# Optimization experiments

Measured on AMD Instinct MI355X. Metric: run time of the kernel, lower is better.

## Reference

```python
import jax, jax.numpy as jnp
import numpy as np


def _linear_init(key, fan_in, fan_out):
    bound = 1.0 / np.sqrt(fan_in)
    k1, k2 = jax.random.split(key)
    w = jax.random.uniform(k1, (fan_in, fan_out), jnp.float32, -bound, bound)
    b = jax.random.uniform(k2, (fan_out,), jnp.float32, -bound, bound)
    return w, b


def setup_inputs() -> dict:
    key = jax.random.key(0)
    ks = jax.random.split(key, 8)
    B, T, K, F, H, D = 4, 64, 50, 6, 128, 256
    states = jax.random.normal(ks[0], (B, T, K, F), jnp.float32)
    masks = (jax.random.uniform(ks[1], (B, T, K)) < 0.9).astype(jnp.float32)
    w_a, b_a = _linear_init(ks[2], F, H)              # agent_encoder
    w_r1, b_r1 = _linear_init(ks[3], 2 * H + 3, H)    # relation_encoder layer 1
    w_r2, b_r2 = _linear_init(ks[4], H, H)            # relation_encoder layer 2
    w_g, b_g = _linear_init(ks[5], 2 * H, H)          # graph_aggregation
    w_f1, b_f1 = _linear_init(ks[6], H, D)            # final_encoder layer 1
    w_f2, b_f2 = _linear_init(ks[7], D, D)            # final_encoder layer 2
    return dict(states=states, masks=masks, w_a=w_a, b_a=b_a,
                w_r1=w_r1, b_r1=b_r1, w_r2=w_r2, b_r2=b_r2,
                w_g=w_g, b_g=b_g, w_f1=w_f1, b_f1=b_f1, w_f2=w_f2, b_f2=b_f2)


def _safe_norm(r):
    # sqrt(sum r^2) with well-defined gradient at 0 (torch.norm convention)
    sq = jnp.sum(r * r, axis=-1, keepdims=True)
    return jnp.where(sq == 0, 0.0, jnp.sqrt(jnp.where(sq == 0, 1.0, sq)))


def reference(states, masks, w_a, b_a, w_r1, b_r1, w_r2, b_r2,
              w_g, b_g, w_f1, b_f1, w_f2, b_f2):
    B, T, K, F = states.shape
    H = w_a.shape[1]
    s = states.reshape(B * T, K, F)            # [N,K,F]
    m = masks.reshape(B * T, K)                # [N,K]
    agent_feat = jax.nn.relu(s @ w_a + b_a)    # [N,K,H] (dropout = identity, eval)
    pos = s[..., :2]
    vel = s[..., 2:4]
    # rel[n,i,j] = quantity_j - quantity_i
    rel_pos = pos[:, None, :, :] - pos[:, :, None, :]   # [N,K,K,2]
    rel_vel = vel[:, None, :, :] - vel[:, :, None, :]
    dist = _safe_norm(rel_pos)                          # [N,K,K,1]
    rx, ry = rel_pos[..., 0:1], rel_pos[..., 1:2]
    safe_x = jnp.where((rx == 0) & (ry == 0), 1.0, rx)  # atan2(0,1)=atan2(0,0)=0
    angle = jnp.arctan2(ry, safe_x)
    speed_diff = _safe_norm(rel_vel)
    geo = jnp.concatenate([dist, angle, speed_diff], axis=-1)  # [N,K,K,3]
    # Split the first relation linear instead of materializing the
    # [N,K,K,2H+3] concat: cat([f_i, f_j, geo]) @ w_r1 == f@w_i + f@w_j + geo@w_geo
    x_i = agent_feat @ w_r1[:H]            # [N,K,H]
    x_j = agent_feat @ w_r1[H:2 * H]       # [N,K,H]
    g = geo @ w_r1[2 * H:] + b_r1          # [N,K,K,H]
    h = jax.nn.relu(x_i[:, :, None, :] + x_j[:, None, :, :] + g)
    rel_feat = h @ w_r2 + b_r2             # [N,K,K,H]
    mask_pairs = m[:, :, None] * m[:, None, :]          # [N,i,j]
    rel_feat = rel_feat * mask_pairs[..., None]
    denom = jnp.maximum(mask_pairs.sum(axis=2, keepdims=True), 1.0)  # [N,K,1]
    agg = rel_feat.sum(axis=2) / denom                  # [N,K,H]
    combined = jax.nn.relu(agent_feat @ w_g[:H] + agg @ w_g[H:] + b_g)  # [N,K,H]
    me = m[..., None]
    pooled = (combined * me).sum(axis=1) / jnp.maximum(me.sum(axis=1), 1.0)  # [N,H]
    latent = jax.nn.relu(pooled @ w_f1 + b_f1) @ w_f2 + b_f2                 # [N,D]
    return latent.reshape(B, T, -1)
```

## Files before the change

kernel.cpp:

```cpp
#include <hip/hip_runtime.h>

#define KA 50
#define KP 52
#define H 128
#define D 256
#define NBLK 256
#define BLOCK 1024
#define NG 8
#define RPT 7
#define STRD 136

#define WS_WI 0
#define WS_WJ 32
#define WS_WR2 64
#define WS_WG 96
#define NFRAG 160

typedef __attribute__((ext_vector_type(8))) short bf16x8;
typedef __attribute__((ext_vector_type(4))) float f32x4;
typedef __attribute__((ext_vector_type(2))) float v2f;

__device__ __forceinline__ float bf2f(unsigned short u) {
  return __uint_as_float(((unsigned)u) << 16);
}
__device__ __forceinline__ unsigned short f2bf_rne(float f) {
  unsigned u = __float_as_uint(f);
  u = (u + 0x7FFFu + ((u >> 16) & 1u)) >> 16;
  return (unsigned short)u;
}
__device__ __forceinline__ unsigned short f2bf(float f) {
  return (unsigned short)((__float_as_uint(f) + 0x8000u) >> 16);
}
__device__ __forceinline__ int rli(int v, int l) {
  return __builtin_amdgcn_readlane(v, l);
}
__device__ __forceinline__ float fast_atan2(float y, float x) {
  const float ax = fabsf(x), ay = fabsf(y);
  const float mx = fmaxf(ax, ay), mn = fminf(ax, ay);
  const float r  = mn * __builtin_amdgcn_rcpf(mx);
  const float r2 = r * r;
  float p = fmaf(r2, 0.0208351f, -0.0851330f);
  p = fmaf(r2, p, 0.1801410f);
  p = fmaf(r2, p, -0.3302995f);
  p = fmaf(r2, p, 0.9998660f);
  float th = r * p;
  if (ay > ax) th = 1.57079632679f - th;
  if (x < 0.f) th = 3.14159265359f - th;
  return copysignf(th, y);
}

__global__ void pack_weights(const float* __restrict__ w_r1,
                             const float* __restrict__ w_r2,
                             const float* __restrict__ w_g,
                             unsigned short* __restrict__ wp) {
  const int t = blockIdx.x * 256 + threadIdx.x;
  if (t >= NFRAG * 64) return;
  const int f = t >> 6, lane = t & 63;
  const float* W; int rowbase, sf;
  if (f < 64)       { W = w_r1; rowbase = (f < 32) ? 0 : 128; sf = f & 31; }
  else if (f < 96)  { W = w_r2; rowbase = 0; sf = f - 64; }
  else              { W = w_g;  rowbase = 0; sf = f - 96; }
  const int kt = sf >> 3, ctl = sf & 7;
  const int col = ctl * 16 + (lane & 15);
  const int k0  = rowbase + kt * 32 + (lane >> 4) * 8;
  unsigned short v[8];
  #pragma unroll
  for (int j = 0; j < 8; ++j) v[j] = f2bf_rne(W[(k0 + j) * H + col]);
  #pragma unroll
  for (int j = 0; j < 8; ++j) wp[(size_t)t * 8 + j] = v[j];
}

struct alignas(16) Smem {
  unsigned short af[KP * STRD];
  unsigned short xi[KP * STRD];
  unsigned short xj[KP * H];
  unsigned short hsum[KP * STRD];
  float red[1024];
  float pooled[H];
  float latent1[D];
  float s[KA][6];
  float m[64];
  float cnta[KP];
  float invden[KP];
  float cnt;
};

__global__ void __launch_bounds__(BLOCK) rpe_kernel(
    const float* __restrict__ states, const float* __restrict__ masks,
    const float* __restrict__ w_a,  const float* __restrict__ b_a,
    const float* __restrict__ w_r1, const float* __restrict__ b_r1,
    const float* __restrict__ b_r2,
    const float* __restrict__ b_g,
    const float* __restrict__ w_f1, const float* __restrict__ b_f1,
    const float* __restrict__ w_f2, const float* __restrict__ b_f2,
    const unsigned short* __restrict__ wp,
    float* __restrict__ out) {
  __shared__ Smem sh;
  const int n = blockIdx.x;
  const int tid = threadIdx.x;
  const int c = tid & (H - 1);
  const int bg = tid >> 7;
  const int wid = tid >> 6, lane = tid & 63;
  const int ct = wid & 7;
  const int rtb = (wid >> 3) * 2;
  const int fr = lane & 15;
  const int fkg = lane >> 4;
  const int col = ct * 16 + fr;

  const float bac = b_a[c];
  const float wa0 = w_a[0*H+c], wa1 = w_a[1*H+c], wa2 = w_a[2*H+c];
  const float wa3 = w_a[3*H+c], wa4 = w_a[4*H+c], wa5 = w_a[5*H+c];
  const int c0 = 2 * lane;
  const v2f wgd01  = { w_r1[256*H + c0], w_r1[256*H + c0+1] };
  const v2f wgan01 = { w_r1[257*H + c0], w_r1[257*H + c0+1] };
  const v2f wgs01  = { w_r1[258*H + c0], w_r1[258*H + c0+1] };
  const v2f br101  = { b_r1[c0], b_r1[c0+1] };

  {
    if (tid < KA * 6) ((float*)sh.s)[tid] = states[(size_t)n * (KA * 6) + tid];
    if (tid < 64) sh.m[tid] = (tid < KA) ? masks[(size_t)n * KA + tid] : 0.f;
    if (tid < 2 * H) {
      const int r5 = KA + (tid >> 7), cc = tid & (H - 1);
      sh.af[r5 * STRD + cc] = 0;
      sh.hsum[r5 * STRD + cc] = 0;
    }
  }
  __syncthreads();
  if (wid == 0) {
    float v = sh.m[lane];
    v += __shfl_xor(v, 1);  v += __shfl_xor(v, 2);  v += __shfl_xor(v, 4);
    v += __shfl_xor(v, 8);  v += __shfl_xor(v, 16); v += __shfl_xor(v, 32);
    if (lane == 0) sh.cnt = v;
  }

  const int bl = (lane < KA) ? lane : (KA - 1);
  const float pbx = sh.s[bl][0], pby = sh.s[bl][1];
  const float pvx = sh.s[bl][2], pvy = sh.s[bl][3];
  const unsigned mbits = (sh.m[lane] != 0.f) ? 0x3F800000u : 0u;
  unsigned q0[3], q1[3];
  #pragma unroll
  for (int r = 0; r < 3; ++r) {
    const int ar = wid + 16 * r;
    const float rx  = pbx - sh.s[ar][0], ry  = pby - sh.s[ar][1];
    const float dvx = pvx - sh.s[ar][2], dvy = pvy - sh.s[ar][3];
    const float dist = sqrtf(fmaf(rx, rx, ry * ry));
    const float sx = (rx == 0.f && ry == 0.f) ? 1.f : rx;
    const float ang = fast_atan2(ry, sx);
    const float sd  = sqrtf(fmaf(dvx, dvx, dvy * dvy));
    q0[r] = (unsigned)f2bf(dist) | ((unsigned)f2bf(ang) << 16);
    q1[r] = (unsigned)f2bf(sd) | mbits;
  }
  unsigned q0t = 0, q1t = 0;
  if (wid < 2) {
    const int ar = 48 + wid;
    const float rx  = pbx - sh.s[ar][0], ry  = pby - sh.s[ar][1];
    const float dvx = pvx - sh.s[ar][2], dvy = pvy - sh.s[ar][3];
    const float dist = sqrtf(fmaf(rx, rx, ry * ry));
    const float sx = (rx == 0.f && ry == 0.f) ? 1.f : rx;
    const float ang = fast_atan2(ry, sx);
    const float sd  = sqrtf(fmaf(dvx, dvx, dvy * dvy));
    q0t = (unsigned)f2bf(dist) | ((unsigned)f2bf(ang) << 16);
    q1t = (unsigned)f2bf(sd) | mbits;
  }

  {
    #pragma unroll
    for (int r = 0; r < RPT; ++r) {
      const int a = bg + NG * r;
      if (a < KA) {
        const float* srow = sh.s[a];
        float v = fmaf(srow[0], wa0, fmaf(srow[1], wa1, fmaf(srow[2], wa2,
                  fmaf(srow[3], wa3, fmaf(srow[4], wa4, fmaf(srow[5], wa5, bac))))));
        sh.af[a * STRD + c] = f2bf(fmaxf(v, 0.f));
      }
    }
  }
  bf16x8 Bi[4], Bj[4];
  #pragma unroll
  for (int kt = 0; kt < 4; ++kt) {
    Bi[kt] = *(const bf16x8*)&wp[(size_t)((WS_WI + kt*8 + ct) * 64 + lane) * 8];
    Bj[kt] = *(const bf16x8*)&wp[(size_t)((WS_WJ + kt*8 + ct) * 64 + lane) * 8];
  }
  __syncthreads();
  if (tid < KP) {
    const float ca = (tid < KA) ? sh.m[tid] * sh.cnt : 0.f;
    sh.cnta[tid] = ca;
    sh.invden[tid] = 1.0f / fmaxf(ca, 1.0f);
  }

  {
    f32x4 ci0 = {0,0,0,0}, ci1 = {0,0,0,0}, cj0 = {0,0,0,0}, cj1 = {0,0,0,0};
    #pragma unroll
    for (int kt = 0; kt < 4; ++kt) {
      const bf16x8 A0 = *(const bf16x8*)&sh.af[(rtb*16 + fr) * STRD + kt*32 + fkg*8];
      const bf16x8 A1 = *(const bf16x8*)&sh.af[((rtb+1)*16 + fr) * STRD + kt*32 + fkg*8];
      ci0 = __builtin_amdgcn_mfma_f32_16x16x32_bf16(A0, Bi[kt], ci0, 0, 0, 0);
      ci1 = __builtin_amdgcn_mfma_f32_16x16x32_bf16(A1, Bi[kt], ci1, 0, 0, 0);
      cj0 = __builtin_amdgcn_mfma_f32_16x16x32_bf16(A0, Bj[kt], cj0, 0, 0, 0);
      cj1 = __builtin_amdgcn_mfma_f32_16x16x32_bf16(A1, Bj[kt], cj1, 0, 0, 0);
    }
    #pragma unroll
    for (int rt2 = 0; rt2 < 2; ++rt2) {
      const f32x4 vi = rt2 ? ci1 : ci0;
      const f32x4 vj = rt2 ? cj1 : cj0;
      #pragma unroll
      for (int g = 0; g < 4; ++g) {
        const int r = (rtb + rt2) * 16 + fkg * 4 + g;
        if (r < KP) {
          sh.xi[r * STRD + col] = f2bf(vi[g]);
          sh.xj[r * H + col]    = f2bf(vj[g]);
        }
      }
    }
  }
  __syncthreads();

  {
    v2f base01[3], acc01[3];
    #pragma unroll
    for (int r = 0; r < 3; ++r) {
      const int ar = wid + 16 * r;
      const unsigned xip = *(const unsigned*)&sh.xi[ar * STRD + c0];
      base01[r] = (v2f){ bf2f((unsigned short)xip), bf2f((unsigned short)(xip >> 16)) } + br101;
      acc01[r] = (v2f){0.f, 0.f};
    }
    #pragma unroll 10
    for (int b = 0; b < KA; ++b) {
      const unsigned xjp = *(const unsigned*)&sh.xj[b * H + c0];
      const v2f xj01 = { __uint_as_float(xjp << 16),
                         __uint_as_float(xjp & 0xFFFF0000u) };
      #pragma unroll
      for (int r = 0; r < 3; ++r) {
        const unsigned rq0 = (unsigned)rli((int)q0[r], b);
        const unsigned rq1 = (unsigned)rli((int)q1[r], b);
        const float dd = __uint_as_float(rq0 << 16);
        const float aa = __uint_as_float(rq0 & 0xFFFF0000u);
        const float ss = __uint_as_float(rq1 << 16);
        const float mm = __uint_as_float(rq1 & 0xFFFF0000u);
        v2f t = __builtin_elementwise_fma((v2f){dd, dd}, wgd01, base01[r] + xj01);
        t = __builtin_elementwise_fma((v2f){aa, aa}, wgan01, t);
        t = __builtin_elementwise_fma((v2f){ss, ss}, wgs01, t);
        t = __builtin_elementwise_max(t, (v2f){0.f, 0.f});
        acc01[r] = __builtin_elementwise_fma((v2f){mm, mm}, t, acc01[r]);
      }
    }
    #pragma unroll
    for (int r = 0; r < 3; ++r) {
      const int ar = wid + 16 * r;
      const float ma = sh.m[ar];
      *(unsigned*)&sh.hsum[ar * STRD + c0] =
          (unsigned)f2bf(acc01[r].x * ma) | ((unsigned)f2bf(acc01[r].y * ma) << 16);
    }
    if (wid < 2) {
      const int ar = 48 + wid;
      const unsigned xip = *(const unsigned*)&sh.xi[ar * STRD + c0];
      const v2f baset = (v2f){ bf2f((unsigned short)xip),
                               bf2f((unsigned short)(xip >> 16)) } + br101;
      v2f acct = {0.f, 0.f};
      #pragma unroll 10
      for (int b = 0; b < KA; ++b) {
        const unsigned xjp = *(const unsigned*)&sh.xj[b * H + c0];
        const v2f xj01 = { __uint_as_float(xjp << 16),
                           __uint_as_float(xjp & 0xFFFF0000u) };
        const unsigned rq0 = (unsigned)rli((int)q0t, b);
        const unsigned rq1 = (unsigned)rli((int)q1t, b);
        const float dd = __uint_as_float(rq0 << 16);
        const float aa = __uint_as_float(rq0 & 0xFFFF0000u);
        const float ss = __uint_as_float(rq1 << 16);
        const float mm = __uint_as_float(rq1 & 0xFFFF0000u);
        v2f t = __builtin_elementwise_fma((v2f){dd, dd}, wgd01, baset + xj01);
        t = __builtin_elementwise_fma((v2f){aa, aa}, wgan01, t);
        t = __builtin_elementwise_fma((v2f){ss, ss}, wgs01, t);
        t = __builtin_elementwise_max(t, (v2f){0.f, 0.f});
        acct = __builtin_elementwise_fma((v2f){mm, mm}, t, acct);
      }
      const float ma = sh.m[ar];
      *(unsigned*)&sh.hsum[ar * STRD + c0] =
          (unsigned)f2bf(acct.x * ma) | ((unsigned)f2bf(acct.y * ma) << 16);
    }
  }
  __syncthreads();

  f32x4 p0 = {0,0,0,0}, p1 = {0,0,0,0};
  {
    f32x4 a0 = {0,0,0,0}, a1 = {0,0,0,0};
    #pragma unroll
    for (int kt = 0; kt < 4; ++kt) {
      const bf16x8 B4 = *(const bf16x8*)&wp[(size_t)((WS_WR2 + kt*8 + ct) * 64 + lane) * 8];
      const bf16x8 A0h = *(const bf16x8*)&sh.hsum[(rtb*16 + fr) * STRD + kt*32 + fkg*8];
      const bf16x8 A1h = *(const bf16x8*)&sh.hsum[((rtb+1)*16 + fr) * STRD + kt*32 + fkg*8];
      a0 = __builtin_amdgcn_mfma_f32_16x16x32_bf16(A0h, B4, a0, 0, 0, 0);
      a1 = __builtin_amdgcn_mfma_f32_16x16x32_bf16(A1h, B4, a1, 0, 0, 0);
      const bf16x8 B5 = *(const bf16x8*)&wp[(size_t)((WS_WG + kt*8 + ct) * 64 + lane) * 8];
      const bf16x8 A0a = *(const bf16x8*)&sh.af[(rtb*16 + fr) * STRD + kt*32 + fkg*8];
      const bf16x8 A1a = *(const bf16x8*)&sh.af[((rtb+1)*16 + fr) * STRD + kt*32 + fkg*8];
      p0 = __builtin_amdgcn_mfma_f32_16x16x32_bf16(A0a, B5, p0, 0, 0, 0);
      p1 = __builtin_amdgcn_mfma_f32_16x16x32_bf16(A1a, B5, p1, 0, 0, 0);
    }
    const float br2c = b_r2[col];
    #pragma unroll
    for (int rt2 = 0; rt2 < 2; ++rt2) {
      const f32x4 v = rt2 ? a1 : a0;
      #pragma unroll
      for (int g = 0; g < 4; ++g) {
        const int r = (rtb + rt2) * 16 + fkg * 4 + g;
        if (r < KP) {
          const float val = fmaf(sh.cnta[r], br2c, v[g]) * sh.invden[r];
          sh.xi[r * STRD + col] = f2bf(val);
        }
      }
    }
  }
  __syncthreads();

  {
    #pragma unroll
    for (int kt = 0; kt < 4; ++kt) {
      const bf16x8 B = *(const bf16x8*)&wp[(size_t)((WS_WG + (kt+4)*8 + ct) * 64 + lane) * 8];
      const bf16x8 A0 = *(const bf16x8*)&sh.xi[(rtb*16 + fr) * STRD + kt*32 + fkg*8];
      const bf16x8 A1 = *(const bf16x8*)&sh.xi[((rtb+1)*16 + fr) * STRD + kt*32 + fkg*8];
      p0 = __builtin_amdgcn_mfma_f32_16x16x32_bf16(A0, B, p0, 0, 0, 0);
      p1 = __builtin_amdgcn_mfma_f32_16x16x32_bf16(A1, B, p1, 0, 0, 0);
    }
    const float bgc = b_g[col];
    float pv = 0.f;
    #pragma unroll
    for (int rt2 = 0; rt2 < 2; ++rt2) {
      const f32x4 v = rt2 ? p1 : p0;
      #pragma unroll
      for (int g = 0; g < 4; ++g) {
        const int r = (rtb + rt2) * 16 + fkg * 4 + g;
        if (r < KA) {
          pv = fmaf(sh.m[r], fmaxf(v[g] + bgc, 0.f), pv);
        }
      }
    }
    pv += __shfl_xor(pv, 16);
    pv += __shfl_xor(pv, 32);
    if (lane < 16) sh.red[(wid >> 3) * H + col] = pv;
  }
  __syncthreads();
  if (tid < H) {
    const float invp = 1.0f / fmaxf(sh.cnt, 1.0f);
    sh.pooled[tid] = (sh.red[tid] + sh.red[H + tid]) * invp;
  }
  __syncthreads();

  {
    const int d  = tid & (D - 1);
    const int hh = tid >> 8;
    const float* wf = w_f1 + d;
    float acc = 0.f;
    const int k0 = hh * 32;
    #pragma unroll 8
    for (int k = 0; k < 32; ++k)
      acc = fmaf(sh.pooled[k0 + k], wf[(k0 + k) * D], acc);
    sh.red[hh * D + d] = acc;
  }
  __syncthreads();
  if (tid < D) {
    sh.latent1[tid] = fmaxf(sh.red[tid] + sh.red[D + tid] +
                            sh.red[2*D + tid] + sh.red[3*D + tid] +
                            b_f1[tid], 0.f);
  }
  __syncthreads();

  {
    const int d  = tid & (D - 1);
    const int hh = tid >> 8;
    const float* wf = w_f2 + d;
    float acc = 0.f;
    const int k0 = hh * 64;
    #pragma unroll 8
    for (int k = 0; k < 64; ++k)
      acc = fmaf(sh.latent1[k0 + k], wf[(k0 + k) * D], acc);
    sh.red[hh * D + d] = acc;
  }
  __syncthreads();
  if (tid < D) {
    out[(size_t)n * D + tid] = sh.red[tid] + sh.red[D + tid] +
                               sh.red[2*D + tid] + sh.red[3*D + tid] +
                               b_f2[tid];
  }
}

extern "C" void kernel_launch(void* const* d_in, const int* in_sizes, int n_in,
                              void* d_out, int out_size, void* d_ws, size_t ws_size,
                              hipStream_t stream) {
  const float* states = (const float*)d_in[0];
  const float* masks  = (const float*)d_in[1];
  const float* w_a  = (const float*)d_in[2];
  const float* b_a  = (const float*)d_in[3];
  const float* w_r1 = (const float*)d_in[4];
  const float* b_r1 = (const float*)d_in[5];
  const float* w_r2 = (const float*)d_in[6];
  const float* b_r2 = (const float*)d_in[7];
  const float* w_g  = (const float*)d_in[8];
  const float* b_g  = (const float*)d_in[9];
  const float* w_f1 = (const float*)d_in[10];
  const float* b_f1 = (const float*)d_in[11];
  const float* w_f2 = (const float*)d_in[12];
  const float* b_f2 = (const float*)d_in[13];
  float* out = (float*)d_out;
  unsigned short* wp = (unsigned short*)d_ws;

  hipLaunchKernelGGL(pack_weights, dim3((NFRAG * 64 + 255) / 256), dim3(256), 0, stream,
                     w_r1, w_r2, w_g, wp);
  hipLaunchKernelGGL(rpe_kernel, dim3(NBLK), dim3(BLOCK), 0, stream,
                     states, masks, w_a, b_a, w_r1, b_r1, b_r2,
                     b_g, w_f1, b_f1, w_f2, b_f2, wp, out);
}
```

Baseline: 37.18 us.

## Split tail-row pair loop across eight waves and fold pooled normalization into MLP

The two leftover agent rows (48, 49) used to be handled by two waves looping over all 50 neighbours while the other 14 waves idled. Now 8 waves each take a 12-13 neighbour chunk of one tail row. Their partial sums are reduced through shared memory after an extra barrier. The separate pooled-vector stage and its barrier are also removed by folding the two-way sum and 1/count scale into the first final-encoder matvec, using the xi buffer as scratch.

```diff
diff --git a/kernel.cpp b/kernel.cpp
--- a/kernel.cpp
+++ b/kernel.cpp
@@ -76,7 +76,6 @@
   unsigned short xj[KP * H];
   unsigned short hsum[KP * STRD];
   float red[1024];
-  float pooled[H];
   float latent1[D];
   float s[KA][6];
   float m[64];
@@ -84,6 +83,58 @@
   float invden[KP];
   float cnt;
 };
+
+__device__ __forceinline__ void ph3_main(const Smem& sh, const unsigned* q0,
+                                         const unsigned* q1, const v2f* base01,
+                                         v2f* acc01, v2f wgd01, v2f wgan01,
+                                         v2f wgs01, int c0) {
+  #pragma unroll 10
+  for (int b = 0; b < KA; ++b) {
+    const unsigned xjp = *(const unsigned*)&sh.xj[b * H + c0];
+    const v2f xj01 = { __uint_as_float(xjp << 16),
+                       __uint_as_float(xjp & 0xFFFF0000u) };
+    #pragma unroll
+    for (int r = 0; r < 3; ++r) {
+      const unsigned rq0 = (unsigned)rli((int)q0[r], b);
+      const unsigned rq1 = (unsigned)rli((int)q1[r], b);
+      const float dd = __uint_as_float(rq0 << 16);
+      const float aa = __uint_as_float(rq0 & 0xFFFF0000u);
+      const float ss = __uint_as_float(rq1 << 16);
+      const float mm = __uint_as_float(rq1 & 0xFFFF0000u);
+      v2f t = __builtin_elementwise_fma((v2f){dd, dd}, wgd01, base01[r] + xj01);
+      t = __builtin_elementwise_fma((v2f){aa, aa}, wgan01, t);
+      t = __builtin_elementwise_fma((v2f){ss, ss}, wgs01, t);
+      t = __builtin_elementwise_max(t, (v2f){0.f, 0.f});
+      acc01[r] = __builtin_elementwise_fma((v2f){mm, mm}, t, acc01[r]);
+    }
+  }
+}
+
+template <int LEN>
+__device__ __forceinline__ void ph3_tail(const Smem& sh, int bbeg,
+                                         unsigned q0t, unsigned q1t,
+                                         v2f baset, v2f& acct,
+                                         v2f wgd01, v2f wgan01, v2f wgs01,
+                                         int c0) {
+  #pragma unroll
+  for (int bi = 0; bi < LEN; ++bi) {
+    const int b = bbeg + bi;
+    const unsigned xjp = *(const unsigned*)&sh.xj[b * H + c0];
+    const v2f xj01 = { __uint_as_float(xjp << 16),
+                       __uint_as_float(xjp & 0xFFFF0000u) };
+    const unsigned rq0 = (unsigned)rli((int)q0t, b);
+    const unsigned rq1 = (unsigned)rli((int)q1t, b);
+    const float dd = __uint_as_float(rq0 << 16);
+    const float aa = __uint_as_float(rq0 & 0xFFFF0000u);
+    const float ss = __uint_as_float(rq1 << 16);
+    const float mm = __uint_as_float(rq1 & 0xFFFF0000u);
+    v2f t = __builtin_elementwise_fma((v2f){dd, dd}, wgd01, baset + xj01);
+    t = __builtin_elementwise_fma((v2f){aa, aa}, wgan01, t);
+    t = __builtin_elementwise_fma((v2f){ss, ss}, wgs01, t);
+    t = __builtin_elementwise_max(t, (v2f){0.f, 0.f});
+    acct = __builtin_elementwise_fma((v2f){mm, mm}, t, acct);
+  }
+}
 
 __global__ void __launch_bounds__(BLOCK) rpe_kernel(
     const float* __restrict__ states, const float* __restrict__ masks,
@@ -137,7 +188,11 @@
   const float pbx = sh.s[bl][0], pby = sh.s[bl][1];
   const float pvx = sh.s[bl][2], pvy = sh.s[bl][3];
   const unsigned mbits = (sh.m[lane] != 0.f) ? 0x3F800000u : 0u;
-  unsigned q0[3], q1[3];
+  const bool hastail = (wid < 8);
+  const int ar4 = 48 + (wid & 1);
+  const int chunk = wid >> 1;
+  const int bbeg = (chunk < 2) ? chunk * 13 : 26 + (chunk - 2) * 12;
+  unsigned q0[3], q1[3], q0t = 0, q1t = 0;
   #pragma unroll
   for (int r = 0; r < 3; ++r) {
     const int ar = wid + 16 * r;
@@ -150,9 +205,8 @@
     q0[r] = (unsigned)f2bf(dist) | ((unsigned)f2bf(ang) << 16);
     q1[r] = (unsigned)f2bf(sd) | mbits;
   }
-  unsigned q0t = 0, q1t = 0;
-  if (wid < 2) {
-    const int ar = 48 + wid;
+  if (hastail) {
+    const int ar = ar4;
     const float rx  = pbx - sh.s[ar][0], ry  = pby - sh.s[ar][1];
     const float dvx = pvx - sh.s[ar][2], dvy = pvy - sh.s[ar][3];
     const float dist = sqrtf(fmaf(rx, rx, ry * ry));
@@ -224,26 +278,7 @@
       base01[r] = (v2f){ bf2f((unsigned short)xip), bf2f((unsigned short)(xip >> 16)) } + br101;
       acc01[r] = (v2f){0.f, 0.f};
     }
-    #pragma unroll 10
-    for (int b = 0; b < KA; ++b) {
-      const unsigned xjp = *(const unsigned*)&sh.xj[b * H + c0];
-      const v2f xj01 = { __uint_as_float(xjp << 16),
-                         __uint_as_float(xjp & 0xFFFF0000u) };
-      #pragma unroll
-      for (int r = 0; r < 3; ++r) {
-        const unsigned rq0 = (unsigned)rli((int)q0[r], b);
-        const unsigned rq1 = (unsigned)rli((int)q1[r], b);
-        const float dd = __uint_as_float(rq0 << 16);
-        const float aa = __uint_as_float(rq0 & 0xFFFF0000u);
-        const float ss = __uint_as_float(rq1 << 16);
-        const float mm = __uint_as_float(rq1 & 0xFFFF0000u);
-        v2f t = __builtin_elementwise_fma((v2f){dd, dd}, wgd01, base01[r] + xj01);
-        t = __builtin_elementwise_fma((v2f){aa, aa}, wgan01, t);
-        t = __builtin_elementwise_fma((v2f){ss, ss}, wgs01, t);
-        t = __builtin_elementwise_max(t, (v2f){0.f, 0.f});
-        acc01[r] = __builtin_elementwise_fma((v2f){mm, mm}, t, acc01[r]);
-      }
-    }
+    ph3_main(sh, q0, q1, base01, acc01, wgd01, wgan01, wgs01, c0);
     #pragma unroll
     for (int r = 0; r < 3; ++r) {
       const int ar = wid + 16 * r;
@@ -251,33 +286,24 @@
       *(unsigned*)&sh.hsum[ar * STRD + c0] =
           (unsigned)f2bf(acc01[r].x * ma) | ((unsigned)f2bf(acc01[r].y * ma) << 16);
     }
-    if (wid < 2) {
-      const int ar = 48 + wid;
-      const unsigned xip = *(const unsigned*)&sh.xi[ar * STRD + c0];
+    if (hastail) {
+      const unsigned xip = *(const unsigned*)&sh.xi[ar4 * STRD + c0];
       const v2f baset = (v2f){ bf2f((unsigned short)xip),
                                bf2f((unsigned short)(xip >> 16)) } + br101;
       v2f acct = {0.f, 0.f};
-      #pragma unroll 10
-      for (int b = 0; b < KA; ++b) {
-        const unsigned xjp = *(const unsigned*)&sh.xj[b * H + c0];
-        const v2f xj01 = { __uint_as_float(xjp << 16),
-                           __uint_as_float(xjp & 0xFFFF0000u) };
-        const unsigned rq0 = (unsigned)rli((int)q0t, b);
-        const unsigned rq1 = (unsigned)rli((int)q1t, b);
-        const float dd = __uint_as_float(rq0 << 16);
-        const float aa = __uint_as_float(rq0 & 0xFFFF0000u);
-        const float ss = __uint_as_float(rq1 << 16);
-        const float mm = __uint_as_float(rq1 & 0xFFFF0000u);
-        v2f t = __builtin_elementwise_fma((v2f){dd, dd}, wgd01, baset + xj01);
-        t = __builtin_elementwise_fma((v2f){aa, aa}, wgan01, t);
-        t = __builtin_elementwise_fma((v2f){ss, ss}, wgs01, t);
-        t = __builtin_elementwise_max(t, (v2f){0.f, 0.f});
-        acct = __builtin_elementwise_fma((v2f){mm, mm}, t, acct);
-      }
-      const float ma = sh.m[ar];
-      *(unsigned*)&sh.hsum[ar * STRD + c0] =
-          (unsigned)f2bf(acct.x * ma) | ((unsigned)f2bf(acct.y * ma) << 16);
-    }
+      if (chunk < 2) ph3_tail<13>(sh, bbeg, q0t, q1t, baset, acct, wgd01, wgan01, wgs01, c0);
+      else           ph3_tail<12>(sh, bbeg, q0t, q1t, baset, acct, wgd01, wgan01, wgs01, c0);
+      *(float2*)&sh.red[wid * H + c0] = make_float2(acct.x, acct.y);
+    }
+  }
+  __syncthreads();
+  if (tid < 256) {
+    const int rr = tid >> 7;
+    const int cc = tid & 127;
+    const float v = ((sh.red[rr * H + cc]       + sh.red[(rr + 2) * H + cc]) +
+                     (sh.red[(rr + 4) * H + cc] + sh.red[(rr + 6) * H + cc])) *
+                    sh.m[48 + rr];
+    sh.hsum[(48 + rr) * STRD + cc] = f2bf(v);
   }
   __syncthreads();
 
@@ -340,41 +366,36 @@
     if (lane < 16) sh.red[(wid >> 3) * H + col] = pv;
   }
   __syncthreads();
-  if (tid < H) {
+
+  float* scr = (float*)sh.xi;
+  const int d67 = tid & (D - 1);
+  const int hh67 = tid >> 8;
+  {
     const float invp = 1.0f / fmaxf(sh.cnt, 1.0f);
-    sh.pooled[tid] = (sh.red[tid] + sh.red[H + tid]) * invp;
-  }
-  __syncthreads();
-
-  {
-    const int d  = tid & (D - 1);
-    const int hh = tid >> 8;
-    const float* wf = w_f1 + d;
+    const float* wf = w_f1 + d67;
     float acc = 0.f;
-    const int k0 = hh * 32;
+    const int k0 = hh67 * 32;
     #pragma unroll 8
     for (int k = 0; k < 32; ++k)
-      acc = fmaf(sh.pooled[k0 + k], wf[(k0 + k) * D], acc);
-    sh.red[hh * D + d] = acc;
+      acc = fmaf(sh.red[k0 + k] + sh.red[H + k0 + k], wf[(k0 + k) * D], acc);
+    scr[hh67 * D + d67] = acc * invp;
   }
   __syncthreads();
   if (tid < D) {
-    sh.latent1[tid] = fmaxf(sh.red[tid] + sh.red[D + tid] +
-                            sh.red[2*D + tid] + sh.red[3*D + tid] +
+    sh.latent1[tid] = fmaxf(scr[tid] + scr[D + tid] +
+                            scr[2*D + tid] + scr[3*D + tid] +
                             b_f1[tid], 0.f);
   }
   __syncthreads();
 
   {
-    const int d  = tid & (D - 1);
-    const int hh = tid >> 8;
-    const float* wf = w_f2 + d;
+    const float* wf = w_f2 + d67;
     float acc = 0.f;
-    const int k0 = hh * 64;
+    const int k0 = hh67 * 64;
     #pragma unroll 8
     for (int k = 0; k < 64; ++k)
       acc = fmaf(sh.latent1[k0 + k], wf[(k0 + k) * D], acc);
-    sh.red[hh * D + d] = acc;
+    sh.red[hh67 * D + d67] = acc;
   }
   __syncthreads();
   if (tid < D) {
```

After: 37.16 us. Within noise of the previous version (-0.1%).
